# Performance work log

Hardware: AMD Instinct MI355X
Metric: run time of the kernel (lower is better)

Reference implementation:

```python
import jax, jax.numpy as jnp
import numpy as np

D = 1024
M = 256
BATCH = 2048


def setup_inputs() -> dict:
    key = jax.random.key(0)
    kx, kw, kp = jax.random.split(key, 3)
    x = jax.random.uniform(kx, (BATCH, D), dtype=jnp.float32)
    W = jax.random.normal(kw, (M,), dtype=jnp.float32)
    P = jax.random.normal(kp, (M, D), dtype=jnp.float32)
    return {"x": x, "W": W, "P": P}


def reference(x, W, P):
    # log mixture weights: log softmax over m
    logw = jax.nn.log_softmax(W, axis=-1)              # [m]
    p = jax.nn.sigmoid(P)                              # [m, d]
    # broadcast Bernoulli likelihood: [batch, m, d]
    lik = x[:, None, :] * p[None, :, :] + (1.0 - x[:, None, :]) * (1.0 - p[None, :, :])
    # per-component log-likelihood summed over features, plus log weight
    comp_ll = jnp.sum(jnp.log(lik), axis=-1) + logw[None, :]   # [batch, m]
    # mixture log-likelihood via logsumexp over components
    return jax.scipy.special.logsumexp(comp_ll, axis=-1)       # [batch]
```

## Files before the change

### kernel.cpp

```cpp
#include <hip/hip_runtime.h>

#define BATCH 2048
#define MM    256
#define DD    1024

#define BB 128
#define BM 64
#define KC 16
#define TB 8
#define TM 4
#define LXS (BB + 4)
#define LRS (BM + 4)

#define LOG2E 1.4426950408889634f
#define LN2   0.6931471805599453f

__device__ __forceinline__ float fr_mant(float x) {
#if __has_builtin(__builtin_amdgcn_frexp_mantf)
    return __builtin_amdgcn_frexp_mantf(x);
#else
    unsigned u = __float_as_uint(x);
    return __uint_as_float((u & 0x807FFFFFu) | 0x3F000000u);
#endif
}
__device__ __forceinline__ int fr_exp(float x) {
#if __has_builtin(__builtin_amdgcn_frexp_expf)
    return __builtin_amdgcn_frexp_expf(x);
#else
    return (int)((__float_as_uint(x) >> 23) & 0xFFu) - 126;
#endif
}

__global__ __launch_bounds__(256) void precomp_kernel(
        const float* __restrict__ P, const float* __restrict__ Wv,
        float* __restrict__ rbuf, float* __restrict__ cst) {
    const int m = blockIdx.x;
    const int t = threadIdx.x;
    const int lane = t & 63, wid = t >> 6;

    float4 z = ((const float4*)(P + (size_t)m * DD))[t];
    float e0 = __expf(z.x), e1 = __expf(z.y), e2 = __expf(z.z), e3 = __expf(z.w);
    ((float4*)(rbuf + (size_t)m * DD))[t] =
        make_float4(e0 - 1.f, e1 - 1.f, e2 - 1.f, e3 - 1.f);
    float part = -(__log2f(1.f + e0) + __log2f(1.f + e1) +
                   __log2f(1.f + e2) + __log2f(1.f + e3));

    __shared__ float smA[4], smB[4];

    #pragma unroll
    for (int o = 32; o; o >>= 1) part += __shfl_xor(part, o);
    if (lane == 0) smA[wid] = part;

    float w = Wv[t];
    float mx = w;
    #pragma unroll
    for (int o = 32; o; o >>= 1) mx = fmaxf(mx, __shfl_xor(mx, o));
    if (lane == 0) smB[wid] = mx;
    __syncthreads();

    float rowc = smA[0] + smA[1] + smA[2] + smA[3];
    float gmx  = fmaxf(fmaxf(smB[0], smB[1]), fmaxf(smB[2], smB[3]));

    float se = __expf(w - gmx);
    #pragma unroll
    for (int o = 32; o; o >>= 1) se += __shfl_xor(se, o);
    __syncthreads();
    if (lane == 0) smA[wid] = se;
    __syncthreads();

    if (t == 0) {
        float sum = smA[0] + smA[1] + smA[2] + smA[3];
        cst[m] = rowc + (Wv[m] - gmx) * LOG2E - __log2f(sum);
    }
}

__global__ __launch_bounds__(256, 4) void main_kernel(
        const float* __restrict__ x, const float* __restrict__ rbuf,
        float* __restrict__ pbuf, int dc) {
    __shared__ __align__(16) float lx[KC * LXS];
    __shared__ __align__(16) float lr[KC * LRS];

    const int tid = threadIdx.x;
    const int tx = tid & 15;
    const int ty = tid >> 4;
    const int m0 = blockIdx.x * BM;
    const int b0 = blockIdx.y * BB;
    const int d0 = blockIdx.z * dc;

    float prod[TB][TM];
    int   acce[TB][TM];
    #pragma unroll
    for (int i = 0; i < TB; ++i)
        #pragma unroll
        for (int j = 0; j < TM; ++j) { prod[i][j] = 1.0f; acce[i][j] = 0; }

    for (int c = 0; c < dc / KC; ++c) {
        const int d = d0 + c * KC;
        __syncthreads();
        #pragma unroll
        for (int l = 0; l < 2; ++l) {
            int idx = tid + 256 * l;
            int row = idx >> 2;
            int seg = idx & 3;
            float4 v = *(const float4*)(x + (size_t)(b0 + row) * DD + d + seg * 4);
            lx[(seg * 4 + 0) * LXS + row] = v.x;
            lx[(seg * 4 + 1) * LXS + row] = v.y;
            lx[(seg * 4 + 2) * LXS + row] = v.z;
            lx[(seg * 4 + 3) * LXS + row] = v.w;
        }
        {
            int row = tid >> 2;
            int seg = tid & 3;
            float4 v = *(const float4*)(rbuf + (size_t)(m0 + row) * DD + d + seg * 4);
            lr[(seg * 4 + 0) * LRS + row] = v.x;
            lr[(seg * 4 + 1) * LRS + row] = v.y;
            lr[(seg * 4 + 2) * LRS + row] = v.z;
            lr[(seg * 4 + 3) * LRS + row] = v.w;
        }
        __syncthreads();

        #pragma unroll
        for (int g = 0; g < 2; ++g) {
            #pragma unroll
            for (int s = 0; s < 8; ++s) {
                const int kc = g * 8 + s;
                const float4* xp = (const float4*)&lx[kc * LXS + TB * ty];
                float4 xa = xp[0], xb = xp[1];
                const float4* rp = (const float4*)&lr[kc * LRS + TM * tx];
                float4 rv = rp[0];
                float xf[TB] = {xa.x, xa.y, xa.z, xa.w, xb.x, xb.y, xb.z, xb.w};
                float rf[TM] = {rv.x, rv.y, rv.z, rv.w};
                #pragma unroll
                for (int i = 0; i < TB; ++i)
                    #pragma unroll
                    for (int j = 0; j < TM; ++j)
                        prod[i][j] *= fmaf(xf[i], rf[j], 1.0f);
            }
            #pragma unroll
            for (int i = 0; i < TB; ++i)
                #pragma unroll
                for (int j = 0; j < TM; ++j) {
                    float p = prod[i][j];
                    acce[i][j] += fr_exp(p);
                    prod[i][j] = fr_mant(p);
                }
        }
    }

    float* pb = pbuf + ((size_t)blockIdx.z * BATCH + b0) * MM + m0;
    #pragma unroll
    for (int i = 0; i < TB; ++i)
        #pragma unroll
        for (int j = 0; j < TM; ++j) {
            float v = (float)acce[i][j] + __log2f(prod[i][j]);
            pb[(size_t)(TB * ty + i) * MM + TM * tx + j] = v;
        }
}

__global__ __launch_bounds__(256) void finalize_kernel(
        const float* __restrict__ pbuf, const float* __restrict__ cst,
        float* __restrict__ out, int sd) {
    const int lane = threadIdx.x & 63;
    const int w = threadIdx.x >> 6;
    const int b = blockIdx.x * 4 + w;

    float v0 = cst[lane];
    float v1 = cst[lane + 64];
    float v2 = cst[lane + 128];
    float v3 = cst[lane + 192];

    for (int s = 0; s < sd; ++s) {
        const float* row = pbuf + ((size_t)s * BATCH + b) * MM;
        v0 += row[lane];
        v1 += row[lane + 64];
        v2 += row[lane + 128];
        v3 += row[lane + 192];
    }

    float mx = fmaxf(fmaxf(v0, v1), fmaxf(v2, v3));
    #pragma unroll
    for (int o = 32; o; o >>= 1) mx = fmaxf(mx, __shfl_xor(mx, o));

    float s = exp2f(v0 - mx) + exp2f(v1 - mx) + exp2f(v2 - mx) + exp2f(v3 - mx);
    #pragma unroll
    for (int o = 32; o; o >>= 1) s += __shfl_xor(s, o);

    if (lane == 0) out[b] = LN2 * (mx + __log2f(s));
}

extern "C" void kernel_launch(void* const* d_in, const int* in_sizes, int n_in,
                              void* d_out, int out_size, void* d_ws, size_t ws_size,
                              hipStream_t stream) {
    const float* x  = (const float*)d_in[0];
    const float* Wv = (const float*)d_in[1];
    const float* P  = (const float*)d_in[2];

    float* ws   = (float*)d_ws;
    float* rbuf = ws;
    float* cst  = rbuf + (size_t)MM * DD;
    float* pbuf = cst + MM;

    size_t fixed = ((size_t)MM * DD + MM) * sizeof(float);
    size_t avail = (ws_size > fixed) ? (ws_size - fixed) : 0;
    int sd = 16;
    while (sd > 1 && (size_t)sd * BATCH * MM * sizeof(float) > avail) sd >>= 1;

    precomp_kernel<<<MM, 256, 0, stream>>>(P, Wv, rbuf, cst);
    dim3 gB(MM / BM, BATCH / BB, sd);
    main_kernel<<<gB, 256, 0, stream>>>(x, rbuf, pbuf, DD / sd);
    finalize_kernel<<<BATCH / 4, 256, 0, stream>>>(pbuf, cst, (float*)d_out, sd);
}
```

Before: 106.3 us.

## Prefetch next chunk into registers, remap blocks across XCDs, vectorize finalize

The main kernel now loads the next KC chunk of x and rbuf into registers while the current chunk is being computed, overlapping global loads with compute. The 3D grid is flattened and blocks are remapped so that the four m-tiles sharing one (b,d) x-tile land on the same XCD, which is meant to improve L2 reuse of x. Output stores to pbuf become float4 writes, and a specialized finalize kernel for sd=16 reads pbuf with float4 loads and a fully unrolled loop. The prefetch costs extra registers, which could lower occupancy under launch_bounds(256,4). The remap assumes a block count that is a multiple of 32 and eight XCDs.

New measurement: 105.8 us. No clear change (-0.4%).

```diff
diff --git a/kernel.cpp b/kernel.cpp
--- a/kernel.cpp
+++ b/kernel.cpp
@@ -11,6 +11,7 @@
 #define TM 4
 #define LXS (BB + 4)
 #define LRS (BM + 4)
+#define NBT (BATCH / BB)
 
 #define LOG2E 1.4426950408889634f
 #define LN2   0.6931471805599453f
@@ -83,9 +84,28 @@
     const int tid = threadIdx.x;
     const int tx = tid & 15;
     const int ty = tid >> 4;
-    const int m0 = blockIdx.x * BM;
-    const int b0 = blockIdx.y * BB;
-    const int d0 = blockIdx.z * dc;
+
+    const int gid  = blockIdx.x;
+    const int xcd  = gid & 7;
+    const int k    = gid >> 3;
+    const int m_id = k & 3;
+    const int tile = (k >> 2) * 8 + xcd;
+    const int b_id = tile & (NBT - 1);
+    const int d_id = tile / NBT;
+
+    const int m0 = m_id * BM;
+    const int b0 = b_id * BB;
+    const int d0 = d_id * dc;
+    const int NC = dc / KC;
+
+    const int rowx = tid >> 2, segx = tid & 3;
+    const float* xp0 = x + (size_t)(b0 + rowx) * DD + d0 + segx * 4;
+    const float* xp1 = xp0 + (size_t)64 * DD;
+    const float* rp  = rbuf + (size_t)(m0 + rowx) * DD + d0 + segx * 4;
+
+    float4 cx0 = *(const float4*)xp0;
+    float4 cx1 = *(const float4*)xp1;
+    float4 cr  = *(const float4*)rp;
 
     float prod[TB][TM];
     int   acce[TB][TM];
@@ -94,28 +114,30 @@
         #pragma unroll
         for (int j = 0; j < TM; ++j) { prod[i][j] = 1.0f; acce[i][j] = 0; }
 
-    for (int c = 0; c < dc / KC; ++c) {
-        const int d = d0 + c * KC;
+    for (int c = 0; c < NC; ++c) {
         __syncthreads();
-        #pragma unroll
-        for (int l = 0; l < 2; ++l) {
-            int idx = tid + 256 * l;
-            int row = idx >> 2;
-            int seg = idx & 3;
-            float4 v = *(const float4*)(x + (size_t)(b0 + row) * DD + d + seg * 4);
-            lx[(seg * 4 + 0) * LXS + row] = v.x;
-            lx[(seg * 4 + 1) * LXS + row] = v.y;
-            lx[(seg * 4 + 2) * LXS + row] = v.z;
-            lx[(seg * 4 + 3) * LXS + row] = v.w;
+        {
+            const int base = segx * 4;
+            lx[(base + 0) * LXS + rowx] = cx0.x;
+            lx[(base + 1) * LXS + rowx] = cx0.y;
+            lx[(base + 2) * LXS + rowx] = cx0.z;
+            lx[(base + 3) * LXS + rowx] = cx0.w;
+            lx[(base + 0) * LXS + rowx + 64] = cx1.x;
+            lx[(base + 1) * LXS + rowx + 64] = cx1.y;
+            lx[(base + 2) * LXS + rowx + 64] = cx1.z;
+            lx[(base + 3) * LXS + rowx + 64] = cx1.w;
+            if (rowx < BM) {
+                lr[(base + 0) * LRS + rowx] = cr.x;
+                lr[(base + 1) * LRS + rowx] = cr.y;
+                lr[(base + 2) * LRS + rowx] = cr.z;
+                lr[(base + 3) * LRS + rowx] = cr.w;
+            }
         }
-        {
-            int row = tid >> 2;
-            int seg = tid & 3;
-            float4 v = *(const float4*)(rbuf + (size_t)(m0 + row) * DD + d + seg * 4);
-            lr[(seg * 4 + 0) * LRS + row] = v.x;
-            lr[(seg * 4 + 1) * LRS + row] = v.y;
-            lr[(seg * 4 + 2) * LRS + row] = v.z;
-            lr[(seg * 4 + 3) * LRS + row] = v.w;
+        if (c + 1 < NC) {
+            xp0 += KC; xp1 += KC; rp += KC;
+            cx0 = *(const float4*)xp0;
+            cx1 = *(const float4*)xp1;
+            cr  = *(const float4*)rp;
         }
         __syncthreads();
 
@@ -126,8 +148,8 @@
                 const int kc = g * 8 + s;
                 const float4* xp = (const float4*)&lx[kc * LXS + TB * ty];
                 float4 xa = xp[0], xb = xp[1];
-                const float4* rp = (const float4*)&lr[kc * LRS + TM * tx];
-                float4 rv = rp[0];
+                const float4* rpf = (const float4*)&lr[kc * LRS + TM * tx];
+                float4 rv = rpf[0];
                 float xf[TB] = {xa.x, xa.y, xa.z, xa.w, xb.x, xb.y, xb.z, xb.w};
                 float rf[TM] = {rv.x, rv.y, rv.z, rv.w};
                 #pragma unroll
@@ -147,14 +169,42 @@
         }
     }
 
-    float* pb = pbuf + ((size_t)blockIdx.z * BATCH + b0) * MM + m0;
-    #pragma unroll
-    for (int i = 0; i < TB; ++i)
-        #pragma unroll
-        for (int j = 0; j < TM; ++j) {
-            float v = (float)acce[i][j] + __log2f(prod[i][j]);
-            pb[(size_t)(TB * ty + i) * MM + TM * tx + j] = v;
-        }
+    float* pb = pbuf + ((size_t)d_id * BATCH + b0) * MM + m0;
+    #pragma unroll
+    for (int i = 0; i < TB; ++i) {
+        float4 vv;
+        vv.x = (float)acce[i][0] + __log2f(prod[i][0]);
+        vv.y = (float)acce[i][1] + __log2f(prod[i][1]);
+        vv.z = (float)acce[i][2] + __log2f(prod[i][2]);
+        vv.w = (float)acce[i][3] + __log2f(prod[i][3]);
+        *(float4*)&pb[(size_t)(TB * ty + i) * MM + TM * tx] = vv;
+    }
+}
+
+__global__ __launch_bounds__(256) void finalize16_kernel(
+        const float4* __restrict__ pbuf4, const float4* __restrict__ cst4,
+        float* __restrict__ out) {
+    const int lane = threadIdx.x & 63;
+    const int w = threadIdx.x >> 6;
+    const int b = blockIdx.x * 4 + w;
+
+    float4 v = cst4[lane];
+    const float4* pb = pbuf4 + (size_t)b * (MM / 4) + lane;
+    #pragma unroll
+    for (int s = 0; s < 16; ++s) {
+        float4 t = pb[(size_t)s * BATCH * (MM / 4)];
+        v.x += t.x; v.y += t.y; v.z += t.z; v.w += t.w;
+    }
+
+    float mx = fmaxf(fmaxf(v.x, v.y), fmaxf(v.z, v.w));
+    #pragma unroll
+    for (int o = 32; o; o >>= 1) mx = fmaxf(mx, __shfl_xor(mx, o));
+
+    float s = exp2f(v.x - mx) + exp2f(v.y - mx) + exp2f(v.z - mx) + exp2f(v.w - mx);
+    #pragma unroll
+    for (int o = 32; o; o >>= 1) s += __shfl_xor(s, o);
+
+    if (lane == 0) out[b] = LN2 * (mx + __log2f(s));
 }
 
 __global__ __launch_bounds__(256) void finalize_kernel(
@@ -206,7 +256,11 @@
     while (sd > 1 && (size_t)sd * BATCH * MM * sizeof(float) > avail) sd >>= 1;
 
     precomp_kernel<<<MM, 256, 0, stream>>>(P, Wv, rbuf, cst);
-    dim3 gB(MM / BM, BATCH / BB, sd);
-    main_kernel<<<gB, 256, 0, stream>>>(x, rbuf, pbuf, DD / sd);
-    finalize_kernel<<<BATCH / 4, 256, 0, stream>>>(pbuf, cst, (float*)d_out, sd);
-}
+    int nblocks = NBT * sd * 4;
+    main_kernel<<<nblocks, 256, 0, stream>>>(x, rbuf, pbuf, DD / sd);
+    if (sd == 16)
+        finalize16_kernel<<<BATCH / 4, 256, 0, stream>>>(
+            (const float4*)pbuf, (const float4*)cst, (float*)d_out);
+    else
+        finalize_kernel<<<BATCH / 4, 256, 0, stream>>>(pbuf, cst, (float*)d_out, sd);
+}
```

## Pre-swizzle tiles, load via global_load_lds, pack FMA, store bf16 partials

Applied to the files above, without the earlier changes.

Adds a swizzle kernel that transposes x and the precomputed ratio buffer into contiguous per-tile layouts. The main kernel can then fill shared memory with direct global-to-LDS loads over a full 64-wide depth chunk with a single sync. The inner product uses packed two-wide float ops, and partial log-likelihoods are stored as bf16 to halve partial-buffer traffic in the finalize pass. This adds an extra transpose pass over x and introduces bf16 rounding error in the partial sums.

After: 111.4 us. 1.05x slower.

```diff
diff --git a/kernel.cpp b/kernel.cpp
--- a/kernel.cpp
+++ b/kernel.cpp
@@ -6,29 +6,37 @@
 
 #define BB 128
 #define BM 64
-#define KC 16
-#define TB 8
-#define TM 4
-#define LXS (BB + 4)
-#define LRS (BM + 4)
+#define DC 64
+#define SD (DD / DC)
+#define NBT (BATCH / BB)
+#define XS_TILE (DC * BB)
+#define RS_TILE (DC * BM)
 
 #define LOG2E 1.4426950408889634f
 #define LN2   0.6931471805599453f
 
+typedef float v2f __attribute__((ext_vector_type(2)));
+
 __device__ __forceinline__ float fr_mant(float x) {
-#if __has_builtin(__builtin_amdgcn_frexp_mantf)
     return __builtin_amdgcn_frexp_mantf(x);
-#else
-    unsigned u = __float_as_uint(x);
-    return __uint_as_float((u & 0x807FFFFFu) | 0x3F000000u);
-#endif
 }
 __device__ __forceinline__ int fr_exp(float x) {
-#if __has_builtin(__builtin_amdgcn_frexp_expf)
     return __builtin_amdgcn_frexp_expf(x);
-#else
-    return (int)((__float_as_uint(x) >> 23) & 0xFFu) - 126;
-#endif
+}
+
+__device__ __forceinline__ unsigned short f2bf(float f) {
+    unsigned u = __float_as_uint(f);
+    u += 0x7FFFu + ((u >> 16) & 1u);
+    return (unsigned short)(u >> 16);
+}
+__device__ __forceinline__ float bf2f(unsigned short u) {
+    return __uint_as_float((unsigned)u << 16);
+}
+
+__device__ __forceinline__ void gl_lds16(const float* g, float* l) {
+    __builtin_amdgcn_global_load_lds(
+        (const __attribute__((address_space(1))) unsigned int*)g,
+        (__attribute__((address_space(3))) unsigned int*)l, 16, 0, 0);
 }
 
 __global__ __launch_bounds__(256) void precomp_kernel(
@@ -74,114 +82,169 @@
     }
 }
 
-__global__ __launch_bounds__(256, 4) void main_kernel(
+__global__ __launch_bounds__(256) void swz_kernel(
         const float* __restrict__ x, const float* __restrict__ rbuf,
-        float* __restrict__ pbuf, int dc) {
-    __shared__ __align__(16) float lx[KC * LXS];
-    __shared__ __align__(16) float lr[KC * LRS];
-
+        float* __restrict__ xs, float* __restrict__ rs) {
+    __shared__ float t[128 * 65];
     const int tid = threadIdx.x;
+    const int bx = blockIdx.x, by = blockIdx.y;
+
+    const float* src;
+    float* dst;
+    int rows;
+    if (bx < NBT) {
+        rows = BB;
+        src = x + (size_t)bx * BB * DD + by * DC;
+        dst = xs + ((size_t)bx * SD + by) * XS_TILE;
+    } else {
+        rows = BM;
+        src = rbuf + (size_t)(bx - NBT) * BM * DD + by * DC;
+        dst = rs + ((size_t)(bx - NBT) * SD + by) * RS_TILE;
+    }
+
+    const int nf4 = rows * (DC / 4);
+    for (int k = 0; k < nf4 / 256; ++k) {
+        int idx4 = tid + 256 * k;
+        int row = idx4 >> 4;
+        int c4  = idx4 & 15;
+        float4 v = *(const float4*)(src + (size_t)row * DD + c4 * 4);
+        t[row * 65 + c4 * 4 + 0] = v.x;
+        t[row * 65 + c4 * 4 + 1] = v.y;
+        t[row * 65 + c4 * 4 + 2] = v.z;
+        t[row * 65 + c4 * 4 + 3] = v.w;
+    }
+    __syncthreads();
+    const int r4 = rows >> 2;
+    for (int k = 0; k < nf4 / 256; ++k) {
+        int o4 = tid + 256 * k;
+        int kc  = o4 / r4;
+        int br4 = o4 - kc * r4;
+        float4 w;
+        w.x = t[(br4 * 4 + 0) * 65 + kc];
+        w.y = t[(br4 * 4 + 1) * 65 + kc];
+        w.z = t[(br4 * 4 + 2) * 65 + kc];
+        w.w = t[(br4 * 4 + 3) * 65 + kc];
+        ((float4*)dst)[o4] = w;
+    }
+}
+
+__global__ __launch_bounds__(256, 3) void main_kernel(
+        const float* __restrict__ xs, const float* __restrict__ rs,
+        unsigned short* __restrict__ pbuf) {
+    __shared__ __align__(16) float lx[XS_TILE];
+    __shared__ __align__(16) float lr[RS_TILE];
+
+    const int tid  = threadIdx.x;
+    const int lane = tid & 63;
+    const int wv   = tid >> 6;
     const int tx = tid & 15;
     const int ty = tid >> 4;
-    const int m0 = blockIdx.x * BM;
-    const int b0 = blockIdx.y * BB;
-    const int d0 = blockIdx.z * dc;
-
-    float prod[TB][TM];
-    int   acce[TB][TM];
-    #pragma unroll
-    for (int i = 0; i < TB; ++i)
-        #pragma unroll
-        for (int j = 0; j < TM; ++j) { prod[i][j] = 1.0f; acce[i][j] = 0; }
-
-    for (int c = 0; c < dc / KC; ++c) {
-        const int d = d0 + c * KC;
-        __syncthreads();
-        #pragma unroll
-        for (int l = 0; l < 2; ++l) {
-            int idx = tid + 256 * l;
-            int row = idx >> 2;
-            int seg = idx & 3;
-            float4 v = *(const float4*)(x + (size_t)(b0 + row) * DD + d + seg * 4);
-            lx[(seg * 4 + 0) * LXS + row] = v.x;
-            lx[(seg * 4 + 1) * LXS + row] = v.y;
-            lx[(seg * 4 + 2) * LXS + row] = v.z;
-            lx[(seg * 4 + 3) * LXS + row] = v.w;
+    const int m_id = blockIdx.x;
+    const int b_id = blockIdx.y;
+    const int d_id = blockIdx.z;
+
+    const float* xg = xs + ((size_t)b_id * SD + d_id) * XS_TILE;
+    const float* rg = rs + ((size_t)m_id * SD + d_id) * RS_TILE;
+
+    #pragma unroll
+    for (int k = 0; k < 8; ++k) {
+        const int off = (wv * 8 + k) * 256;
+        gl_lds16(xg + off + lane * 4, lx + off);
+    }
+    #pragma unroll
+    for (int k = 0; k < 4; ++k) {
+        const int off = (wv * 4 + k) * 256;
+        gl_lds16(rg + off + lane * 4, lr + off);
+    }
+
+    const v2f one2 = {1.0f, 1.0f};
+    v2f prod[4][4];
+    int acce[8][4];
+    #pragma unroll
+    for (int i2 = 0; i2 < 4; ++i2)
+        #pragma unroll
+        for (int j = 0; j < 4; ++j) prod[i2][j] = one2;
+    #pragma unroll
+    for (int i = 0; i < 8; ++i)
+        #pragma unroll
+        for (int j = 0; j < 4; ++j) acce[i][j] = 0;
+
+    __syncthreads();
+
+    const float4* xa = (const float4*)(lx + 8 * ty);
+    const float4* rb = (const float4*)(lr + 4 * tx);
+
+    #pragma unroll
+    for (int g = 0; g < 8; ++g) {
+        #pragma unroll
+        for (int s = 0; s < 8; ++s) {
+            const int kc = g * 8 + s;
+            float4 x0 = xa[kc * 32];
+            float4 x1 = xa[kc * 32 + 1];
+            float4 rv = rb[kc * 16];
+            v2f xp2[4] = {{x0.x, x0.y}, {x0.z, x0.w},
+                          {x1.x, x1.y}, {x1.z, x1.w}};
+            float rf[4] = {rv.x, rv.y, rv.z, rv.w};
+            #pragma unroll
+            for (int j = 0; j < 4; ++j) {
+                v2f rr = {rf[j], rf[j]};
+                #pragma unroll
+                for (int i2 = 0; i2 < 4; ++i2) {
+                    v2f tt = __builtin_elementwise_fma(xp2[i2], rr, one2);
+                    prod[i2][j] = prod[i2][j] * tt;
+                }
+            }
         }
-        {
-            int row = tid >> 2;
-            int seg = tid & 3;
-            float4 v = *(const float4*)(rbuf + (size_t)(m0 + row) * DD + d + seg * 4);
-            lr[(seg * 4 + 0) * LRS + row] = v.x;
-            lr[(seg * 4 + 1) * LRS + row] = v.y;
-            lr[(seg * 4 + 2) * LRS + row] = v.z;
-            lr[(seg * 4 + 3) * LRS + row] = v.w;
+        #pragma unroll
+        for (int i2 = 0; i2 < 4; ++i2)
+            #pragma unroll
+            for (int j = 0; j < 4; ++j) {
+                v2f p = prod[i2][j];
+                acce[2 * i2 + 0][j] += fr_exp(p.x);
+                acce[2 * i2 + 1][j] += fr_exp(p.y);
+                p.x = fr_mant(p.x);
+                p.y = fr_mant(p.y);
+                prod[i2][j] = p;
+            }
+    }
+
+    unsigned short* pb = pbuf + ((size_t)d_id * BATCH + (size_t)b_id * BB) * MM
+                              + (size_t)m_id * BM;
+    #pragma unroll
+    for (int i2 = 0; i2 < 4; ++i2)
+        #pragma unroll
+        for (int h = 0; h < 2; ++h) {
+            const int i = 2 * i2 + h;
+            float f0 = (float)acce[i][0] + __log2f(h ? prod[i2][0].y : prod[i2][0].x);
+            float f1 = (float)acce[i][1] + __log2f(h ? prod[i2][1].y : prod[i2][1].x);
+            float f2 = (float)acce[i][2] + __log2f(h ? prod[i2][2].y : prod[i2][2].x);
+            float f3 = (float)acce[i][3] + __log2f(h ? prod[i2][3].y : prod[i2][3].x);
+            ushort4 w;
+            w.x = f2bf(f0); w.y = f2bf(f1); w.z = f2bf(f2); w.w = f2bf(f3);
+            *(ushort4*)&pb[(size_t)(8 * ty + i) * MM + 4 * tx] = w;
         }
-        __syncthreads();
-
-        #pragma unroll
-        for (int g = 0; g < 2; ++g) {
-            #pragma unroll
-            for (int s = 0; s < 8; ++s) {
-                const int kc = g * 8 + s;
-                const float4* xp = (const float4*)&lx[kc * LXS + TB * ty];
-                float4 xa = xp[0], xb = xp[1];
-                const float4* rp = (const float4*)&lr[kc * LRS + TM * tx];
-                float4 rv = rp[0];
-                float xf[TB] = {xa.x, xa.y, xa.z, xa.w, xb.x, xb.y, xb.z, xb.w};
-                float rf[TM] = {rv.x, rv.y, rv.z, rv.w};
-                #pragma unroll
-                for (int i = 0; i < TB; ++i)
-                    #pragma unroll
-                    for (int j = 0; j < TM; ++j)
-                        prod[i][j] *= fmaf(xf[i], rf[j], 1.0f);
-            }
-            #pragma unroll
-            for (int i = 0; i < TB; ++i)
-                #pragma unroll
-                for (int j = 0; j < TM; ++j) {
-                    float p = prod[i][j];
-                    acce[i][j] += fr_exp(p);
-                    prod[i][j] = fr_mant(p);
-                }
-        }
-    }
-
-    float* pb = pbuf + ((size_t)blockIdx.z * BATCH + b0) * MM + m0;
-    #pragma unroll
-    for (int i = 0; i < TB; ++i)
-        #pragma unroll
-        for (int j = 0; j < TM; ++j) {
-            float v = (float)acce[i][j] + __log2f(prod[i][j]);
-            pb[(size_t)(TB * ty + i) * MM + TM * tx + j] = v;
-        }
 }
 
 __global__ __launch_bounds__(256) void finalize_kernel(
-        const float* __restrict__ pbuf, const float* __restrict__ cst,
-        float* __restrict__ out, int sd) {
+        const unsigned short* __restrict__ pbuf, const float* __restrict__ cst,
+        float* __restrict__ out) {
     const int lane = threadIdx.x & 63;
     const int w = threadIdx.x >> 6;
     const int b = blockIdx.x * 4 + w;
 
-    float v0 = cst[lane];
-    float v1 = cst[lane + 64];
-    float v2 = cst[lane + 128];
-    float v3 = cst[lane + 192];
-
-    for (int s = 0; s < sd; ++s) {
-        const float* row = pbuf + ((size_t)s * BATCH + b) * MM;
-        v0 += row[lane];
-        v1 += row[lane + 64];
-        v2 += row[lane + 128];
-        v3 += row[lane + 192];
-    }
-
-    float mx = fmaxf(fmaxf(v0, v1), fmaxf(v2, v3));
+    float4 v = ((const float4*)cst)[lane];
+    const ushort4* pb = (const ushort4*)pbuf + (size_t)b * (MM / 4) + lane;
+    #pragma unroll
+    for (int s = 0; s < SD; ++s) {
+        ushort4 t = pb[(size_t)s * BATCH * (MM / 4)];
+        v.x += bf2f(t.x); v.y += bf2f(t.y); v.z += bf2f(t.z); v.w += bf2f(t.w);
+    }
+
+    float mx = fmaxf(fmaxf(v.x, v.y), fmaxf(v.z, v.w));
     #pragma unroll
     for (int o = 32; o; o >>= 1) mx = fmaxf(mx, __shfl_xor(mx, o));
 
-    float s = exp2f(v0 - mx) + exp2f(v1 - mx) + exp2f(v2 - mx) + exp2f(v3 - mx);
+    float s = exp2f(v.x - mx) + exp2f(v.y - mx) + exp2f(v.z - mx) + exp2f(v.w - mx);
     #pragma unroll
     for (int o = 32; o; o >>= 1) s += __shfl_xor(s, o);
 
@@ -196,17 +259,16 @@
     const float* P  = (const float*)d_in[2];
 
     float* ws   = (float*)d_ws;
-    float* rbuf = ws;
+    float* xs   = ws;
+    float* rs   = xs + (size_t)NBT * SD * XS_TILE;
+    float* rbuf = rs + (size_t)(MM / BM) * SD * RS_TILE;
     float* cst  = rbuf + (size_t)MM * DD;
-    float* pbuf = cst + MM;
-
-    size_t fixed = ((size_t)MM * DD + MM) * sizeof(float);
-    size_t avail = (ws_size > fixed) ? (ws_size - fixed) : 0;
-    int sd = 16;
-    while (sd > 1 && (size_t)sd * BATCH * MM * sizeof(float) > avail) sd >>= 1;
+    unsigned short* pbuf = (unsigned short*)(cst + MM);
 
     precomp_kernel<<<MM, 256, 0, stream>>>(P, Wv, rbuf, cst);
-    dim3 gB(MM / BM, BATCH / BB, sd);
-    main_kernel<<<gB, 256, 0, stream>>>(x, rbuf, pbuf, DD / sd);
-    finalize_kernel<<<BATCH / 4, 256, 0, stream>>>(pbuf, cst, (float*)d_out, sd);
-}
+    dim3 gS(NBT + MM / BM, SD);
+    swz_kernel<<<gS, 256, 0, stream>>>(x, rbuf, xs, rs);
+    dim3 gB(MM / BM, NBT, SD);
+    main_kernel<<<gB, 256, 0, stream>>>(xs, rs, pbuf);
+    finalize_kernel<<<BATCH / 4, 256, 0, stream>>>(pbuf, cst, (float*)d_out);
+}
```
